# Optimization experiments

Hardware: AMD Instinct MI355X
Metric: run time of the kernel (lower is better)

The kernel has to match this reference:

```python
import jax, jax.numpy as jnp
import numpy as np

# (pt, eta, phi) feature indices per particle for each block (eta=None for MET)
A_PT, A_ETA, A_PHI = [5, 4, 35, 34], [9, 8, 45, 44], [13, 12, 55, 54]            # e3,e2,j9,j8
B_PT, B_ETA, B_PHI = [3, 33, 31, 2], [7, 43, 41, 6], [11, 53, 51, 10]            # e1,j7,j5,e0
C_PT, C_ETA, C_PHI = [28, 32, 15, 16], [38, 42, 19, 20], [48, 52, 23, 24]        # j2,j6,mu1,mu2
D_PT, D_ETA, D_PHI = [0, 14, 30, 26, 29, 27, 17], [None, 18, 40, 36, 39, 37, 21], [1, 22, 50, 46, 49, 47, 25]  # MET,mu0,j4,j0,j3,j1,mu3


def _bc(a, nd):
    # broadcast a (B,) or () angle factor over nd trailing qubit axes
    return a.reshape(a.shape + (1,) * nd)


def _rx(state, theta, w):
    nd = state.ndim - 2
    c = _bc(jnp.cos(theta * 0.5), nd)
    s = _bc(jnp.sin(theta * 0.5), nd)
    s0 = jnp.take(state, 0, axis=w + 1)
    s1 = jnp.take(state, 1, axis=w + 1)
    return jnp.stack([c * s0 - 1j * s * s1, -1j * s * s0 + c * s1], axis=w + 1)


def _ry(state, theta, w):
    nd = state.ndim - 2
    c = _bc(jnp.cos(theta * 0.5), nd)
    s = _bc(jnp.sin(theta * 0.5), nd)
    s0 = jnp.take(state, 0, axis=w + 1)
    s1 = jnp.take(state, 1, axis=w + 1)
    return jnp.stack([c * s0 - s * s1, s * s0 + c * s1], axis=w + 1)


def _rz(state, theta, w):
    nd = state.ndim - 2
    ph = _bc(jnp.exp(-0.5j * theta.astype(state.dtype)), nd)
    s0 = jnp.take(state, 0, axis=w + 1)
    s1 = jnp.take(state, 1, axis=w + 1)
    return jnp.stack([ph * s0, jnp.conj(ph) * s1], axis=w + 1)


def _cnot(state, ctrl, tgt):
    c0 = jnp.take(state, 0, axis=ctrl + 1)
    c1 = jnp.take(state, 1, axis=ctrl + 1)
    t_ax = tgt + 1 if tgt < ctrl else tgt  # ctrl axis removed shifts higher wires down
    c1 = jnp.flip(c1, axis=t_ax)
    return jnp.stack([c0, c1], axis=ctrl + 1)


def _extract(x, pt_idx, eta_idx, phi_idx):
    pt = x[:, np.array(pt_idx)]
    eta = jnp.stack([x[:, i] if i is not None else jnp.zeros(x.shape[0], x.dtype) for i in eta_idx], axis=1)
    phi = x[:, np.array(phi_idx)]
    return pt, eta, phi


def _run_block(pt, eta, phi, weights, n, latent, trash, depth):
    B = pt.shape[0]
    state = jnp.zeros((B,) + (2,) * n, dtype=jnp.complex64)
    state = state.at[(slice(None),) + (0,) * n].set(1.0)
    for k in range(n):
        state = _rx(state, eta[:, k], k)
        state = _ry(state, pt[:, k], k)
        state = _rz(state, phi[:, k], k)
    for k in range(n - 1):
        state = _cnot(state, k, k + 1)
    for k in range(n):
        state = _rz(state, eta[:, k], k)
        state = _ry(state, pt[:, k], k)
        state = _rx(state, phi[:, k], k)
    for d in range(depth):
        for t in trash:
            for l in latent:
                state = _cnot(state, t, l)
        for k in range(n):
            state = _ry(state, weights[d * n + k], k)
        for l in latent:
            for t in trash:
                state = _cnot(state, l, t)
    p = jnp.abs(state) ** 2  # (B, 2,...,2) real probabilities
    red = tuple(range(1, n))
    zs = [jnp.sum(jnp.take(p, 0, axis=w + 1), axis=red) - jnp.sum(jnp.take(p, 1, axis=w + 1), axis=red) for w in trash]
    return jnp.stack(zs, axis=1)


def setup_inputs() -> dict:
    key = jax.random.key(0)
    k0, k1, k2, k3, k4 = jax.random.split(key, 5)
    B = 131072
    x = jax.random.normal(k0, (B, 56), dtype=jnp.float32)
    wA = 0.01 * jax.random.normal(k1, (4,), dtype=jnp.float32)
    wB = 0.01 * jax.random.normal(k2, (4,), dtype=jnp.float32)
    wC = 0.01 * jax.random.normal(k3, (4,), dtype=jnp.float32)
    wD = 0.01 * jax.random.normal(k4, (28,), dtype=jnp.float32)
    return {"x": x, "wA": wA, "wB": wB, "wC": wC, "wD": wD}


def reference(x, wA, wB, wC, wD):
    zA = _run_block(*_extract(x, A_PT, A_ETA, A_PHI), wA, 4, (0, 1), (2, 3), 1)  # (B,2)
    zB = _run_block(*_extract(x, B_PT, B_ETA, B_PHI), wB, 4, (0, 1), (2, 3), 1)  # (B,2)
    zC = _run_block(*_extract(x, C_PT, C_ETA, C_PHI), wC, 4, (0, 1), (2, 3), 1)  # (B,2)
    zD = _run_block(*_extract(x, D_PT, D_ETA, D_PHI), wD, 7, (0, 1, 2, 3), (4, 5, 6), 4)  # (B,3)
    return jnp.concatenate([zA, zB, zC, zD], axis=1)  # (B,9) ~ dict values concatenated
```

## Files before the change

### kernel.cpp

```cpp
#include <hip/hip_runtime.h>
#include <hip/hip_fp16.h>


#define DEVINL __device__ __forceinline__

typedef _Float16 hv2 __attribute__((ext_vector_type(2)));
typedef unsigned int u32;
typedef u32 vreg16 __attribute__((ext_vector_type(16)));
typedef u32 vreg64 __attribute__((ext_vector_type(64)));

struct C2 { __half2 rr, mp; };

DEVINL C2 mkc(float re, float im) {
  C2 c; c.rr = __floats2half2_rn(re, re); c.mp = __floats2half2_rn(-im, im); return c;
}
DEVINL __half2 mkamp(float re, float im) { return __floats2half2_rn(re, im); }
DEVINL __half2 swap2(__half2 v) { return __lowhigh2highlow(v); }
DEVINL __half2 cmulc(C2 u, __half2 v) { return __hfma2(u.rr, v, __hmul2(u.mp, swap2(v))); }

DEVINL float ampsq(__half2 v, float acc) {
#if __has_builtin(__builtin_amdgcn_fdot2)
  return __builtin_amdgcn_fdot2(__builtin_bit_cast(hv2, v), __builtin_bit_cast(hv2, v), acc, false);
#else
  float2 f = __half22float2(v);
  return fmaf(f.x, f.x, fmaf(f.y, f.y, acc));
#endif
}

constexpr int parc(int x) { x ^= x >> 4; x ^= x >> 2; x ^= x >> 1; return x & 1; }

struct c32 { float x, y; };
DEVINL c32 cmulf(c32 a, c32 b) { return { a.x*b.x - a.y*b.y, a.x*b.y + a.y*b.x }; }

template<class VT>
DEVINL __half2 vget(const VT& A, int i) { return __builtin_bit_cast(__half2, (u32)A[i]); }
template<class VT>
DEVINL void vset(VT& A, int i, __half2 v) { A[i] = __builtin_bit_cast(u32, v); }

DEVINL __half2 lx1(__half2 v) {
  int q = __shfl_xor(__builtin_bit_cast(int, v), 1, 64);
  return __builtin_bit_cast(__half2, q);
}
DEVINL float lx1f(float v) { return __shfl_xor(v, 1, 64); }


template<int N, int W, class VT>
DEVINL void g_ry(VT& A, __half2 c2, __half2 s2, __half2 ns2) {
  constexpr int M = 1 << (N - 1 - W);
#pragma unroll
  for (int i = 0; i < (1 << N); ++i) if (!(i & M)) {
    const int j = i | M;
    __half2 v0 = vget(A, i), v1 = vget(A, j);
    vset(A, i, __hfma2(c2, v0, __hmul2(ns2, v1)));
    vset(A, j, __hfma2(c2, v1, __hmul2(s2, v0)));
  }
}

template<int N, int W, class VT>
DEVINL void g_u2(VT& A, C2 u00, C2 u01, C2 u10, C2 u11) {
  constexpr int M = 1 << (N - 1 - W);
#pragma unroll
  for (int i = 0; i < (1 << N); ++i) if (!(i & M)) {
    const int j = i | M;
    __half2 v0 = vget(A, i), v1 = vget(A, j), v0s = swap2(v0), v1s = swap2(v1);
    vset(A, i, __hfma2(u00.rr, v0, __hfma2(u00.mp, v0s, __hfma2(u01.rr, v1, __hmul2(u01.mp, v1s)))));
    vset(A, j, __hfma2(u10.rr, v0, __hfma2(u10.mp, v0s, __hfma2(u11.rr, v1, __hmul2(u11.mp, v1s)))));
  }
}

template<int N, int C, int T, class VT>
DEVINL void g_cnot(VT& A) {
  constexpr int CM = 1 << (N - 1 - C), TM = 1 << (N - 1 - T);
#pragma unroll
  for (int i = 0; i < (1 << N); ++i) if ((i & CM) && !(i & TM)) {
    const int j = i | TM;
    __half2 t = vget(A, i); vset(A, i, vget(A, j)); vset(A, j, t);
  }
}

template<int N, int K, class VT>
DEVINL void chain_cnot(VT& A) {
  if constexpr (K < N - 1) { g_cnot<N, K, K + 1>(A); chain_cnot<N, K + 1>(A); }
}


DEVINL void mk_u01(float ce, float se, float cp, float sp, float cf, float sf,
                   c32& u0, c32& u1) {
  u0 = cmulf({cf, -sf}, {cp * ce, sp * se});
  u1 = cmulf({cf,  sf}, {sp * ce, -cp * se});
}

DEVINL void mk_U(float ce, float se, float cp, float sp, float cf, float sf,
                 C2& U00, C2& U01, C2& U10, C2& U11) {
  c32 z = {ce, -se}, zb = {ce, se};
  c32 A = cmulf({cf * cp, -sf * sp}, z);
  c32 T = cmulf({cf * sp,  sf * cp}, zb);
  c32 Cc = cmulf({cf * sp, -sf * cp}, z);
  c32 D = cmulf({cf * cp,  sf * sp}, zb);
  U00 = mkc(A.x, A.y); U01 = mkc(-T.x, -T.y); U10 = mkc(Cc.x, Cc.y); U11 = mkc(D.x, D.y);
}

DEVINL void load_sc(const float* __restrict__ xr, int eta_i, int pt_i, int phi_i,
                    float& ce, float& se, float& cp, float& sp, float& cf, float& sf) {
  float e = (eta_i < 0) ? 0.f : xr[eta_i];
  __sincosf(0.5f * e, &se, &ce);
  __sincosf(0.5f * xr[pt_i], &sp, &cp);
  __sincosf(0.5f * xr[phi_i], &sf, &cf);
}

template<int N, int M, class VT, class CF>
DEVINL void build_rec(VT& A, CF cf) {
  if constexpr (M < N) {
    c32 u0, u1; cf(M, u0, u1);
    C2 c0 = mkc(u0.x, u0.y), c1 = mkc(u1.x, u1.y);
#pragma unroll
    for (int j = (1 << M) - 1; j >= 0; --j) {
      __half2 s = vget(A, j);
      vset(A, 2 * j,     cmulc(c0, s));
      vset(A, 2 * j + 1, cmulc(c1, s));
    }
    build_rec<N, M + 1>(A, cf);
  }
}

template<int N, int K, class VT, class CF>
DEVINL void usweep_rec(VT& A, CF cf) {
  if constexpr (K < N) {
    C2 U00, U01, U10, U11;
    cf(K, U00, U01, U10, U11);
    g_u2<N, K>(A, U00, U01, U10, U11);
    usweep_rec<N, K + 1>(A, cf);
  }
}

template<int N, int K, class VT, class CF>
DEVINL void ry_rec(VT& A, CF cf) {
  if constexpr (K < N) {
    __half2 c2, s2, ns2;
    cf(K, c2, s2, ns2);
    g_ry<N, K>(A, c2, s2, ns2);
    ry_rec<N, K + 1>(A, cf);
  }
}


template<int I>
DEVINL void sim4h(const float* __restrict__ xr, const float* __restrict__ w, float* z) {
  constexpr int PT[3][4]  = {{5, 4, 35, 34}, {3, 33, 31, 2}, {28, 32, 15, 16}};
  constexpr int ETA[3][4] = {{9, 8, 45, 44}, {7, 43, 41, 6}, {38, 42, 19, 20}};
  constexpr int PHI[3][4] = {{13, 12, 55, 54}, {11, 53, 51, 10}, {48, 52, 23, 24}};
  vreg16 A;
  vset(A, 0, mkamp(1.f, 0.f));
  build_rec<4, 0>(A, [&](int M, c32& u0, c32& u1) {
    float ce, se, cp, sp, cf, sf;
    load_sc(xr, ETA[I][M], PT[I][M], PHI[I][M], ce, se, cp, sp, cf, sf);
    mk_u01(ce, se, cp, sp, cf, sf, u0, u1);
  });
  chain_cnot<4, 0>(A);
  usweep_rec<4, 0>(A, [&](int K, C2& U00, C2& U01, C2& U10, C2& U11) {
    float ce, se, cp, sp, cf, sf;
    load_sc(xr, ETA[I][K], PT[I][K], PHI[I][K], ce, se, cp, sp, cf, sf);
    mk_U(ce, se, cp, sp, cf, sf, U00, U01, U10, U11);
  });

#pragma unroll
  for (int i = 0; i < 16; ++i)
    if (parc(i & 3) && !(i & 8)) {
      __half2 t = vget(A, i); vset(A, i, vget(A, i ^ 12)); vset(A, i ^ 12, t);
    }

  ry_rec<4, 0>(A, [&](int K, __half2& c2, __half2& s2, __half2& ns2) {
    float sv, cv; __sincosf(0.5f * w[K], &sv, &cv);
    c2 = __floats2half2_rn(cv, cv);
    s2 = __floats2half2_rn(sv, sv);
    ns2 = __floats2half2_rn(-sv, -sv);
  });

#pragma unroll
  for (int i = 0; i < 16; ++i)
    if (parc(i & 12) && !(i & 2)) {
      __half2 t = vget(A, i); vset(A, i, vget(A, i ^ 3)); vset(A, i ^ 3, t);
    }

  float cls[4];
#pragma unroll
  for (int c = 0; c < 4; ++c) cls[c] = 0.f;
#pragma unroll
  for (int i = 0; i < 16; ++i) cls[i & 3] = ampsq(vget(A, i), cls[i & 3]);
  float z0 = 0.f, z1 = 0.f;
#pragma unroll
  for (int c = 0; c < 4; ++c) {
    z0 += (c & 2) ? -cls[c] : cls[c];
    z1 += (c & 1) ? -cls[c] : cls[c];
  }
  z[0] = z0; z[1] = z1;
}


DEVINL void role4(const float* __restrict__ x,
                  const float* __restrict__ wA, const float* __restrict__ wB,
                  const float* __restrict__ wC,
                  float* __restrict__ out, int B, int s, int rb) {
  const int b = rb * 256 + threadIdx.x;
  if (b >= B) return;
  const float* xr = x + (size_t)b * 56;

  float o[2];
  if (s == 0)      sim4h<0>(xr, wA, o);
  else if (s == 1) sim4h<1>(xr, wB, o);
  else             sim4h<2>(xr, wC, o);

  float* op = out + (size_t)b * 9 + 2 * s;
  op[0] = o[0]; op[1] = o[1];
}

DEVINL void role7(const float* __restrict__ x, const float* __restrict__ wD,
                  float* __restrict__ out, int B, int rb) {
  const int t = rb * 256 + threadIdx.x;
  const int b = t >> 1;
  if (b >= B) return;
  const bool po = (t & 1) != 0;

  constexpr int PT[7]  = {0, 14, 30, 26, 29, 27, 17};
  constexpr int ETA[7] = {-1, 18, 40, 36, 39, 37, 21};
  constexpr int PHI[7] = {1, 22, 50, 46, 49, 47, 25};

  const float* xr = x + (size_t)b * 56;

  vreg64 A;
  vset(A, 0, mkamp(1.f, 0.f));
  build_rec<6, 0>(A, [&](int M, c32& u0, c32& u1) {
    const int k = M + 1;
    float ce, se, cp, sp, cf, sf;
    load_sc(xr, ETA[k], PT[k], PHI[k], ce, se, cp, sp, cf, sf);
    mk_u01(ce, se, cp, sp, cf, sf, u0, u1);
  });
  {
    float ce, se, cp, sp, cf, sf;
    load_sc(xr, ETA[0], PT[0], PHI[0], ce, se, cp, sp, cf, sf);
    c32 u0, u1; mk_u01(ce, se, cp, sp, cf, sf, u0, u1);
    C2 c0 = mkc(po ? u1.x : u0.x, po ? u1.y : u0.y);
#pragma unroll
    for (int i = 0; i < 64; ++i) vset(A, i, cmulc(c0, vget(A, i)));
  }

#pragma unroll
  for (int i = 0; i < 32; ++i) {
    const int j = i | 32;
    __half2 lo = vget(A, i), hi = vget(A, j);
    vset(A, i, po ? hi : lo);
    vset(A, j, po ? lo : hi);
  }
  chain_cnot<6, 0>(A);

  {
    float ce, se, cp, sp, cf, sf;
    load_sc(xr, ETA[0], PT[0], PHI[0], ce, se, cp, sp, cf, sf);
    C2 U00, U01, U10, U11;
    mk_U(ce, se, cp, sp, cf, sf, U00, U01, U10, U11);
    C2 UA, UB;
    UA.rr = po ? U11.rr : U00.rr; UA.mp = po ? U11.mp : U00.mp;
    UB.rr = po ? U10.rr : U01.rr; UB.mp = po ? U10.mp : U01.mp;
#pragma unroll
    for (int i = 0; i < 64; ++i) {
      __half2 m = vget(A, i), q = lx1(m);
      vset(A, i, __hfma2(UA.rr, m, __hfma2(UA.mp, swap2(m),
                 __hfma2(UB.rr, q, __hmul2(UB.mp, swap2(q))))));
    }
  }
  usweep_rec<6, 0>(A, [&](int W, C2& U00, C2& U01, C2& U10, C2& U11) {
    const int k = W + 1;
    float ce, se, cp, sp, cf, sf;
    load_sc(xr, ETA[k], PT[k], PHI[k], ce, se, cp, sp, cf, sf);
    mk_U(ce, se, cp, sp, cf, sf, U00, U01, U10, U11);
  });

#pragma unroll 1
  for (int d = 0; d < 4; ++d) {
#pragma unroll
    for (int i = 0; i < 64; ++i)
      if (parc(i & 7) && !(i & 0x20)) {
        const int j = i ^ 0x38;
        __half2 t0 = lx1(vget(A, j));
        __half2 t1 = lx1(vget(A, i));
        vset(A, i, t0); vset(A, j, t1);
      }

    {
      float sv, cv; __sincosf(0.5f * wD[7 * d], &sv, &cv);
      __half2 c2v = __floats2half2_rn(cv, cv);
      __half2 sp2 = __floats2half2_rn(po ? sv : -sv, po ? sv : -sv);
#pragma unroll
      for (int i = 0; i < 64; ++i) {
        __half2 q = lx1(vget(A, i));
        vset(A, i, __hfma2(c2v, vget(A, i), __hmul2(sp2, q)));
      }
    }
    ry_rec<6, 0>(A, [&](int W, __half2& c2, __half2& s2, __half2& ns2) {
      float sv, cv; __sincosf(0.5f * wD[7 * d + W + 1], &sv, &cv);
      c2 = __floats2half2_rn(cv, cv);
      s2 = __floats2half2_rn(sv, sv);
      ns2 = __floats2half2_rn(-sv, -sv);
    });

#pragma unroll
    for (int i = 0; i < 64; ++i)
      if (!(i & 4)) {
        const int j = i ^ 7;
        const bool cond = parc(i & 0x38) ? !po : po;
        __half2 lo = vget(A, i), hi = vget(A, j);
        vset(A, i, cond ? hi : lo);
        vset(A, j, cond ? lo : hi);
      }
  }

  float cls[8];
#pragma unroll
  for (int c = 0; c < 8; ++c) cls[c] = 0.f;
#pragma unroll
  for (int i = 0; i < 64; ++i) cls[i & 7] = ampsq(vget(A, i), cls[i & 7]);
  float z4 = 0.f, z5 = 0.f, z6 = 0.f;
#pragma unroll
  for (int c = 0; c < 8; ++c) {
    z4 += (c & 4) ? -cls[c] : cls[c];
    z5 += (c & 2) ? -cls[c] : cls[c];
    z6 += (c & 1) ? -cls[c] : cls[c];
  }
  z4 += lx1f(z4); z5 += lx1f(z5); z6 += lx1f(z6);
  if (!po) {
    float* op = out + (size_t)b * 9 + 6;
    op[0] = z4; op[1] = z5; op[2] = z6;
  }
}


__global__ void
__attribute__((amdgpu_flat_work_group_size(256, 256), amdgpu_waves_per_eu(2, 4)))
k_all(const float* __restrict__ x,
      const float* __restrict__ wA, const float* __restrict__ wB,
      const float* __restrict__ wC, const float* __restrict__ wD,
      float* __restrict__ out, int B, int gx) {
  const int bx = blockIdx.x;
  if (bx < 3 * gx) {
    const int s = (bx >= 2 * gx) ? 2 : (int)(bx >= gx);
    role4(x, wA, wB, wC, out, B, s, bx - s * gx);
  } else {
    role7(x, wD, out, B, bx - 3 * gx);
  }
}


extern "C" void kernel_launch(void* const* d_in, const int* in_sizes, int n_in,
                              void* d_out, int out_size, void* d_ws, size_t ws_size,
                              hipStream_t stream) {
  const float* x  = (const float*)d_in[0];
  const float* wA = (const float*)d_in[1];
  const float* wB = (const float*)d_in[2];
  const float* wC = (const float*)d_in[3];
  const float* wD = (const float*)d_in[4];
  float* out = (float*)d_out;
  const int B = in_sizes[0] / 56;
  const int threads = 256;

  const int gx = (B + threads - 1) / threads;
  const int gy = (2 * B + threads - 1) / threads;
  k_all<<<3 * gx + gy, threads, 0, stream>>>(x, wA, wB, wC, wD, out, B, gx);
}
```

Baseline: 140.0 us.

## Co-locate all sub-circuits for a 64-row chunk in one block

Replaces the grid split by role (separate block ranges for blocks A, B, C and D) with blocks that each handle 64 rows. Within a block, wave 0 runs A and B, wave 3 runs C, and waves 1-2 run the paired 7-qubit D simulation. This keeps each row's x data and output line within one block so cache lines are shared and partial-line writes are combined. The risk is load imbalance: the D waves do much more work than the A/B and C waves, so waves may sit idle inside a block.

Result: slower. 145.8 us (+4.1%).

```diff
diff --git a/kernel.cpp b/kernel.cpp
--- a/kernel.cpp
+++ b/kernel.cpp
@@ -197,35 +197,11 @@
 }
 
 
-DEVINL void role4(const float* __restrict__ x,
-                  const float* __restrict__ wA, const float* __restrict__ wB,
-                  const float* __restrict__ wC,
-                  float* __restrict__ out, int B, int s, int rb) {
-  const int b = rb * 256 + threadIdx.x;
-  if (b >= B) return;
-  const float* xr = x + (size_t)b * 56;
-
-  float o[2];
-  if (s == 0)      sim4h<0>(xr, wA, o);
-  else if (s == 1) sim4h<1>(xr, wB, o);
-  else             sim4h<2>(xr, wC, o);
-
-  float* op = out + (size_t)b * 9 + 2 * s;
-  op[0] = o[0]; op[1] = o[1];
-}
-
-DEVINL void role7(const float* __restrict__ x, const float* __restrict__ wD,
-                  float* __restrict__ out, int B, int rb) {
-  const int t = rb * 256 + threadIdx.x;
-  const int b = t >> 1;
-  if (b >= B) return;
-  const bool po = (t & 1) != 0;
-
+DEVINL void role7(const float* __restrict__ xr, const float* __restrict__ wD,
+                  float* __restrict__ out_row, bool po) {
   constexpr int PT[7]  = {0, 14, 30, 26, 29, 27, 17};
   constexpr int ETA[7] = {-1, 18, 40, 36, 39, 37, 21};
   constexpr int PHI[7] = {1, 22, 50, 46, 49, 47, 25};
-
-  const float* xr = x + (size_t)b * 56;
 
   vreg64 A;
   vset(A, 0, mkamp(1.f, 0.f));
@@ -328,8 +304,7 @@
   }
   z4 += lx1f(z4); z5 += lx1f(z5); z6 += lx1f(z6);
   if (!po) {
-    float* op = out + (size_t)b * 9 + 6;
-    op[0] = z4; op[1] = z5; op[2] = z6;
+    out_row[6] = z4; out_row[7] = z5; out_row[8] = z6;
   }
 }
 
@@ -339,13 +314,34 @@
 k_all(const float* __restrict__ x,
       const float* __restrict__ wA, const float* __restrict__ wB,
       const float* __restrict__ wC, const float* __restrict__ wD,
-      float* __restrict__ out, int B, int gx) {
-  const int bx = blockIdx.x;
-  if (bx < 3 * gx) {
-    const int s = (bx >= 2 * gx) ? 2 : (int)(bx >= gx);
-    role4(x, wA, wB, wC, out, B, s, bx - s * gx);
+      float* __restrict__ out, int B) {
+  const int base = blockIdx.x * 64;
+  const int wv = threadIdx.x >> 6;
+  const int lane = threadIdx.x & 63;
+
+  if (wv == 0) {
+    const int b = base + lane;
+    if (b >= B) return;
+    const float* xr = x + (size_t)b * 56;
+    float o[4];
+    sim4h<0>(xr, wA, &o[0]);
+    sim4h<1>(xr, wB, &o[2]);
+    float* op = out + (size_t)b * 9;
+    op[0] = o[0]; op[1] = o[1]; op[2] = o[2]; op[3] = o[3];
+  } else if (wv == 3) {
+    const int b = base + lane;
+    if (b >= B) return;
+    const float* xr = x + (size_t)b * 56;
+    float o[2];
+    sim4h<2>(xr, wC, o);
+    float* op = out + (size_t)b * 9;
+    op[4] = o[0]; op[5] = o[1];
   } else {
-    role7(x, wD, out, B, bx - 3 * gx);
+    const int p = (wv - 1) * 32 + (lane >> 1);
+    const int b = base + p;
+    if (b >= B) return;
+    const bool po = (lane & 1) != 0;
+    role7(x + (size_t)b * 56, wD, out + (size_t)b * 9, po);
   }
 }
 
@@ -360,9 +356,7 @@
   const float* wD = (const float*)d_in[4];
   float* out = (float*)d_out;
   const int B = in_sizes[0] / 56;
-  const int threads = 256;
-
-  const int gx = (B + threads - 1) / threads;
-  const int gy = (2 * B + threads - 1) / threads;
-  k_all<<<3 * gx + gy, threads, 0, stream>>>(x, wA, wB, wC, wD, out, B, gx);
-}
+
+  const int blocks = (B + 63) / 64;
+  k_all<<<blocks, 256, 0, stream>>>(x, wA, wB, wC, wD, out, B);
+}
```
